# Performance work log

Hardware: AMD Instinct MI355X
Metric: run time of the kernel (lower is better)

Reference implementation:

```python
import jax, jax.numpy as jnp
import numpy as np
from jax.scipy.special import logsumexp

G, H, L, N, K = 2000, 128, 10, 4096, 10
TAU, LC, LA, EPS = 0.1, 1.0, 0.5, 1e-6

def _lin_init(k, fi, fo):
    return jax.random.normal(k, (fi, fo), jnp.float32) / np.sqrt(fi)

def setup_inputs():
    key = jax.random.key(0)
    ks = jax.random.split(key, 12)
    return {
        'wt_x': jax.random.normal(ks[0], (N, G), jnp.float32),
        'ko_x': jax.random.normal(ks[1], (N, G), jnp.float32),
        'wt_labels': jax.random.randint(ks[2], (N,), 0, K, dtype=jnp.int32),
        'ko_labels': jax.random.randint(ks[3], (N,), 0, K, dtype=jnp.int32),
        'enc_w1': _lin_init(ks[4], G, H), 'enc_b1': jnp.zeros((H,)),
        'enc_g': jnp.ones((H,)), 'enc_be': jnp.zeros((H,)),
        'enc_w2': _lin_init(ks[5], H, L), 'enc_b2': jnp.zeros((L,)),
        'kap_w1': _lin_init(ks[6], G, H), 'kap_b1': jnp.zeros((H,)),
        'kap_g': jnp.ones((H,)), 'kap_be': jnp.zeros((H,)),
        'kap_w2': _lin_init(ks[7], H, 1), 'kap_b2': jnp.zeros((1,)),
        'dec_w1': _lin_init(ks[8], L, H), 'dec_b1': jnp.zeros((H,)),
        'dec_g': jnp.ones((H,)), 'dec_be': jnp.zeros((H,)),
        'dec_w2': _lin_init(ks[9], H, G), 'dec_b2': jnp.zeros((G,)),
    }

def _mlp(x, w1, b1, g, be, w2, b2):
    # Linear -> LayerNorm -> ReLU -> Linear (dropout_prob=0)
    h = x @ w1 + b1
    m = h.mean(-1, keepdims=True)
    v = ((h - m) ** 2).mean(-1, keepdims=True)
    h = (h - m) / jnp.sqrt(v + 1e-5) * g + be
    return jax.nn.relu(h) @ w2 + b2

def _contrastive(z_wt, z_ko, y_wt, y_ko):
    S = (z_wt @ z_ko.T) / TAU  # [Nwt, Nko], unit-norm z so |S| <= 1/tau
    total = jnp.float32(0.0)
    n_shared = jnp.float32(0.0)
    for c in range(K):  # fixed small class count
        mwt = (y_wt == c).astype(S.dtype)
        mko = (y_ko == c).astype(S.dtype)
        n_wt, n_ko = mwt.sum(), mko.sum()
        valid = (n_wt > 0) & (n_ko > 0)
        nw, nk = jnp.maximum(n_wt, 1.0), jnp.maximum(n_ko, 1.0)
        # mean_{i in c, j in c} (LSE_i - S_ij) over ko columns of class c
        lse_r = logsumexp(jnp.where(mko[None, :] > 0, S, -1e4), axis=1)
        l1 = jnp.sum(mwt * (lse_r - (S @ mko) / nk)) / nw
        lse_c = logsumexp(jnp.where(mwt[:, None] > 0, S, -1e4), axis=0)
        l2 = jnp.sum(mko * (lse_c - (mwt @ S) / nw)) / nk
        total = total + jnp.where(valid, 0.5 * (l1 + l2), 0.0)
        n_shared = n_shared + valid.astype(S.dtype)
    return jnp.where(n_shared > 0, total / jnp.maximum(n_shared, 1.0), 0.0)

def _alignment(z, y):
    ones = jnp.ones(z.shape[0], z.dtype)
    counts = jax.ops.segment_sum(ones, y, num_segments=K)
    mu_c = jax.ops.segment_sum(z, y, num_segments=K) / jnp.maximum(counts, 1.0)[:, None]
    dev = z - mu_c[y]
    per_class = jax.ops.segment_sum(jnp.sum(dev ** 2, axis=1), y, num_segments=K) / jnp.maximum(counts, 1.0)
    present = counts > 0
    return jnp.sum(jnp.where(present, per_class, 0.0)) / jnp.maximum(jnp.sum(present.astype(z.dtype)), 1.0)

def reference(wt_x, ko_x, enc_w1, enc_b1, enc_g, enc_be, enc_w2, enc_b2, kap_w1, kap_b1, kap_g, kap_be, kap_w2, kap_b2, dec_w1, dec_b1, dec_g, dec_be, dec_w2, dec_b2, wt_labels, ko_labels):
    def encode(x):
        mu = _mlp(x, enc_w1, enc_b1, enc_g, enc_be, enc_w2, enc_b2)
        mu = mu / jnp.maximum(jnp.linalg.norm(mu, axis=1, keepdims=True), 1e-12)
        kappa = jax.nn.softplus(_mlp(x, kap_w1, kap_b1, kap_g, kap_be, kap_w2, kap_b2)) + EPS
        return mu, kappa
    wt_mu, wt_kappa = encode(wt_x)
    ko_mu, ko_kappa = encode(ko_x)
    wt_z, ko_z = wt_mu, ko_mu  # eval mode: z = mu (deterministic)
    wt_rec = _mlp(wt_z, dec_w1, dec_b1, dec_g, dec_be, dec_w2, dec_b2)
    ko_rec = _mlp(ko_z, dec_w1, dec_b1, dec_g, dec_be, dec_w2, dec_b2)
    recon = jnp.mean((wt_rec - wt_x) ** 2) + jnp.mean((ko_rec - ko_x) ** 2)
    kl = (wt_kappa.mean() + ko_kappa.mean()) * 0.01
    contrast = _contrastive(wt_z, ko_z, wt_labels, ko_labels)
    align = _alignment(jnp.concatenate([wt_z, ko_z], 0), jnp.concatenate([wt_labels, ko_labels], 0))
    return recon + kl + LC * contrast + LA * align
```

## Files before the change

kernel.cpp:

```cpp
#include <hip/hip_runtime.h>
#include <math.h>

typedef __attribute__((ext_vector_type(8))) __bf16 bf16x8;
typedef __attribute__((ext_vector_type(4))) float f32x4;

#define GL2LDS_(gptr, lptr) \
    __builtin_amdgcn_global_load_lds((const __attribute__((address_space(1))) void*)(gptr), \
                                     (__attribute__((address_space(3))) void*)(lptr), 16, 0, 0)

#define OFF_NWT   0
#define OFF_NKO   10
#define OFF_L1    20
#define OFF_L2    30
#define OFF_CNT   40
#define OFF_ZSUM  50
#define OFF_ZSQ   150
#define OFF_KSUM  160
#define OFF_REC   162
#define IOFF_WTOFF 192
#define IOFF_KOOFF 204
#define IOFF_WTCTR 216
#define IOFF_KOCTR 226
#define ACC_FLOATS 256

#define WT_OFF    256
#define WTLO_OFF  (WT_OFF + 262144)
#define H_OFF     (WTLO_OFF + 262144)
#define Z_OFF     (H_OFF + 8192*256)
#define KAP_OFF   (Z_OFF + 8192*10)
#define HREST_OFF (KAP_OFF + 8192)
#define HPART     2097152

#define ACT_HI_OFF  H_OFF
#define ACT_LO_OFF  (H_OFF + 524288)
#define BT_HI_OFF   (H_OFF + 1048576)
#define BT_LO_OFF   (H_OFF + 1179648)
#define ZCKO_OFF    (H_OFF + 1310720)
#define ZCWT_OFF    (H_OFF + 1351680)
#define PART_OFF    (H_OFF + 1392640)

__global__ __launch_bounds__(256) void pack_w_kernel(const float* __restrict__ enc_w1,
                                                     const float* __restrict__ kap_w1,
                                                     __bf16* __restrict__ WThi,
                                                     __bf16* __restrict__ WTlo)
{
    __shared__ float tile[64][65];
    int kt = blockIdx.x & 31;
    int ct = blockIdx.x >> 5;
    int k0 = kt * 64, c0 = ct * 64;
    int t = threadIdx.x;
    int lr = t >> 6, lc = t & 63;
#pragma unroll
    for (int i = 0; i < 16; ++i) {
        int k = k0 + lr + 4 * i;
        int c = c0 + lc;
        float v = 0.f;
        if (k < 2000) v = (c < 128) ? enc_w1[(size_t)k * 128 + c]
                                    : kap_w1[(size_t)k * 128 + (c - 128)];
        tile[lc][lr + 4 * i] = v;
    }
    __syncthreads();
#pragma unroll
    for (int i = 0; i < 16; ++i) {
        int c = c0 + lr + 4 * i;
        int k = k0 + lc;
        float v = tile[lr + 4 * i][lc];
        __bf16 h = (__bf16)v;
        __bf16 l = (__bf16)(v - (float)h);
        size_t idx = (size_t)c * 2048 + k;
        WThi[idx] = h;
        WTlo[idx] = l;
    }
}

__global__ __launch_bounds__(256) void pack_dw2_kernel(const float* __restrict__ dw2,
                                                       __bf16* __restrict__ BThi,
                                                       __bf16* __restrict__ BTlo)
{
    __shared__ float tile[64][129];
    int j0 = blockIdx.x * 64;
    int t = threadIdx.x;
#pragma unroll
    for (int i = 0; i < 32; ++i) {
        int idx = i * 256 + t;
        int c = idx >> 6, jj = idx & 63;
        int j = j0 + jj;
        tile[jj][c] = (j < 2000) ? dw2[(size_t)c * 2000 + j] : 0.f;
    }
    __syncthreads();
#pragma unroll
    for (int i = 0; i < 32; ++i) {
        int idx = i * 256 + t;
        int jj = idx >> 7, c = idx & 127;
        float v = tile[jj][c];
        __bf16 h = (__bf16)v;
        size_t o = (size_t)(j0 + jj) * 128 + c;
        BThi[o] = h;
        BTlo[o] = (__bf16)(v - (float)h);
    }
}

__global__ void counts_kernel(const int* __restrict__ wtl, const int* __restrict__ kol,
                              float* __restrict__ acc)
{
    __shared__ int cw[10], ck[10];
    int t = threadIdx.x;
    if (t < 10) { cw[t] = 0; ck[t] = 0; }
    __syncthreads();
    for (int i = t; i < 4096; i += 1024) {
        atomicAdd(&cw[wtl[i]], 1);
        atomicAdd(&ck[kol[i]], 1);
    }
    __syncthreads();
    if (t < 10) { acc[OFF_NWT + t] = (float)cw[t]; acc[OFF_NKO + t] = (float)ck[t]; }
    if (t == 0) {
        int* ai = (int*)acc;
        int aw = 0, ak = 0;
        for (int c = 0; c < 10; ++c) {
            ai[IOFF_WTOFF + c] = aw; aw += cw[c];
            ai[IOFF_KOOFF + c] = ak; ak += ck[c];
        }
        ai[IOFF_WTOFF + 10] = aw;
        ai[IOFF_KOOFF + 10] = ak;
    }
}

__global__ __launch_bounds__(256) void scatter_z_kernel(const float* __restrict__ Z,
                                                        const int* __restrict__ wtl,
                                                        const int* __restrict__ kol,
                                                        float* __restrict__ acc,
                                                        float* __restrict__ ZcWT,
                                                        float* __restrict__ ZcKO)
{
    __shared__ int lcnt[20];
    __shared__ int lbase[20];
    int t = threadIdx.x;
    if (t < 20) lcnt[t] = 0;
    __syncthreads();
    int row = blockIdx.x * 256 + t;
    int side = row >= 4096;
    int r = side ? row - 4096 : row;
    int c = side ? kol[r] : wtl[r];
    int key = side * 10 + c;
    int myrank = atomicAdd(&lcnt[key], 1);
    __syncthreads();
    int* ai = (int*)acc;
    if (t < 20 && lcnt[t] > 0)
        lbase[t] = atomicAdd(&ai[IOFF_WTCTR + t], lcnt[t]);
    __syncthreads();
    int off = side ? ai[IOFF_KOOFF + c] : ai[IOFF_WTOFF + c];
    int slot = off + lbase[key] + myrank;
    float* dst = side ? ZcKO : ZcWT;
    const float* zr = Z + (size_t)row * 10;
#pragma unroll
    for (int d = 0; d < 10; ++d) dst[d * 4096 + slot] = zr[d];
}

__global__ __launch_bounds__(512) void gemm1_kernel(const float* __restrict__ wt_x,
                                                    const float* __restrict__ ko_x,
                                                    const __bf16* __restrict__ WThi,
                                                    const __bf16* __restrict__ WTlo,
                                                    float* __restrict__ Hb,
                                                    float* __restrict__ Hrest,
                                                    int nkc)
{
    __shared__ short Bs[2][2][2][4096];
    int t = threadIdx.x;
    int widx = t >> 6, lane = t & 63;
    int wm = widx >> 1, wn = widx & 1;
    int b = blockIdx.x;
    int mt = b & 63, strip = (b >> 6) & 1, kc = b >> 7;
    int R0 = mt * 128;
    int cb = strip * 128;
    int kchunk = 2048 / nkc;
    int kbase = kc * kchunk;
    int kleft = 2000 - kbase;
    int nsteps = (kleft < kchunk) ? ((kleft + 31) >> 5) : (kchunk >> 5);
    int ntiles = (nsteps + 1) >> 1;

    const float* xb = (R0 < 4096) ? (wt_x + (size_t)R0 * 2000)
                                  : (ko_x + (size_t)(R0 - 4096) * 2000);
    int ar = wm * 32 + (lane & 15);
    const float* xrow0 = xb + (size_t)ar * 2000 + kbase;
    const float* xrow1 = xrow0 + (size_t)16 * 2000;
    int kboff = (lane >> 4) * 8;

    int col0 = t >> 2;
    int s0   = (t & 3) ^ ((col0 >> 1) & 3);
    size_t boff = (size_t)(cb + col0) * 2048 + kbase + s0 * 8;
    const __bf16* bsrcH = WThi + boff;
    const __bf16* bsrcL = WTlo + boff;

#define STAGEB_(buf, tl) do { \
    int st_ = (tl) * 2; \
    GL2LDS_(bsrcH + (size_t)st_ * 32,       &Bs[buf][0][0][t * 8]); \
    GL2LDS_(bsrcH + (size_t)(st_ + 1) * 32, &Bs[buf][0][1][t * 8]); \
    GL2LDS_(bsrcL + (size_t)st_ * 32,       &Bs[buf][1][0][t * 8]); \
    GL2LDS_(bsrcL + (size_t)(st_ + 1) * 32, &Bs[buf][1][1][t * 8]); } while (0)

    f32x4 acc00, acc01, acc02, acc03;
    f32x4 acc10, acc11, acc12, acc13;
#pragma unroll
    for (int r = 0; r < 4; ++r) {
        acc00[r]=0.f; acc01[r]=0.f; acc02[r]=0.f; acc03[r]=0.f;
        acc10[r]=0.f; acc11[r]=0.f; acc12[r]=0.f; acc13[r]=0.f;
    }

    float4 aA00, aA01, aA10, aA11, aA20, aA21, aA30, aA31;
    float4 aB00, aB01, aB10, aB11, aB20, aB21, aB30, aB31;

#define GLOADA_(step, a00, a01, a10, a11) do { \
    int k0_ = (step) * 32; \
    int k_ = k0_ + kboff; \
    if (kbase + k0_ <= 1952) { \
        a00 = *(const float4*)(xrow0 + k_); \
        a01 = *(const float4*)(xrow0 + k_ + 4); \
        a10 = *(const float4*)(xrow1 + k_); \
        a11 = *(const float4*)(xrow1 + k_ + 4); \
    } else { \
        float t0_[8], t1_[8]; \
        _Pragma("unroll") \
        for (int j = 0; j < 8; ++j) { \
            int kk = kbase + k_ + j; \
            t0_[j] = (kk < 2000) ? xrow0[k_ + j] : 0.f; \
            t1_[j] = (kk < 2000) ? xrow1[k_ + j] : 0.f; } \
        a00 = make_float4(t0_[0], t0_[1], t0_[2], t0_[3]); \
        a01 = make_float4(t0_[4], t0_[5], t0_[6], t0_[7]); \
        a10 = make_float4(t1_[0], t1_[1], t1_[2], t1_[3]); \
        a11 = make_float4(t1_[4], t1_[5], t1_[6], t1_[7]); } } while (0)

#define CONVA_(a0, a1, ahi, alo) do { \
    float av_[8] = {a0.x, a0.y, a0.z, a0.w, a1.x, a1.y, a1.z, a1.w}; \
    _Pragma("unroll") \
    for (int j = 0; j < 8; ++j) { \
        __bf16 h_ = (__bf16)av_[j]; \
        ahi[j] = h_; \
        alo[j] = (__bf16)(av_[j] - (float)h_); } } while (0)

#define MFMAH_(buf, half, ahi0, alo0, ahi1, alo1) do { \
    _Pragma("unroll") \
    for (int nf = 0; nf < 4; ++nf) { \
        bf16x8 bhf = *(const bf16x8*)&Bs[buf][0][half][(ubase + nf * 64) * 8]; \
        bf16x8 blf = *(const bf16x8*)&Bs[buf][1][half][(ubase + nf * 64) * 8]; \
        f32x4* a0 = (nf == 0) ? &acc00 : (nf == 1) ? &acc01 : (nf == 2) ? &acc02 : &acc03; \
        f32x4* a1 = (nf == 0) ? &acc10 : (nf == 1) ? &acc11 : (nf == 2) ? &acc12 : &acc13; \
        *a0 = __builtin_amdgcn_mfma_f32_16x16x32_bf16(ahi0, bhf, *a0, 0, 0, 0); \
        *a0 = __builtin_amdgcn_mfma_f32_16x16x32_bf16(alo0, bhf, *a0, 0, 0, 0); \
        *a0 = __builtin_amdgcn_mfma_f32_16x16x32_bf16(ahi0, blf, *a0, 0, 0, 0); \
        *a1 = __builtin_amdgcn_mfma_f32_16x16x32_bf16(ahi1, bhf, *a1, 0, 0, 0); \
        *a1 = __builtin_amdgcn_mfma_f32_16x16x32_bf16(alo1, bhf, *a1, 0, 0, 0); \
        *a1 = __builtin_amdgcn_mfma_f32_16x16x32_bf16(ahi1, blf, *a1, 0, 0, 0); } } while (0)

    STAGEB_(0, 0);
    GLOADA_(0, aA00, aA01, aA10, aA11);
    GLOADA_(1, aA20, aA21, aA30, aA31);
    if (1 < ntiles) {
        GLOADA_(2, aB00, aB01, aB10, aB11);
        GLOADA_(3, aB20, aB21, aB30, aB31);
    }
    __syncthreads();

    int cpr = lane & 15;
    int pph = (lane >> 4) ^ ((cpr >> 1) & 3);
    int ubase = (wn * 64 + cpr) * 4 + pph;

    int half_iters = (ntiles + 1) >> 1;
    for (int it = 0; it < half_iters; ++it) {
        int tl = it * 2;
        {
            if (tl + 1 < ntiles) STAGEB_(1, tl + 1);
            bf16x8 h00,l00,h01,l01,h10,l10,h11,l11;
            CONVA_(aA00, aA01, h00, l00); CONVA_(aA10, aA11, h01, l01);
            CONVA_(aA20, aA21, h10, l10); CONVA_(aA30, aA31, h11, l11);
            if (tl + 2 < ntiles) {
                GLOADA_(2*(tl+2),   aA00, aA01, aA10, aA11);
                GLOADA_(2*(tl+2)+1, aA20, aA21, aA30, aA31);
            }
            MFMAH_(0, 0, h00, l00, h01, l01);
            MFMAH_(0, 1, h10, l10, h11, l11);
            __syncthreads();
        }
        if (tl + 1 < ntiles) {
            if (tl + 2 < ntiles) STAGEB_(0, tl + 2);
            bf16x8 h00,l00,h01,l01,h10,l10,h11,l11;
            CONVA_(aB00, aB01, h00, l00); CONVA_(aB10, aB11, h01, l01);
            CONVA_(aB20, aB21, h10, l10); CONVA_(aB30, aB31, h11, l11);
            if (tl + 3 < ntiles) {
                GLOADA_(2*(tl+3),   aB00, aB01, aB10, aB11);
                GLOADA_(2*(tl+3)+1, aB20, aB21, aB30, aB31);
            }
            MFMAH_(1, 0, h00, l00, h01, l01);
            MFMAH_(1, 1, h10, l10, h11, l11);
            __syncthreads();
        }
    }

    float* Hq = (kc == 0) ? Hb : (Hrest + (size_t)(kc - 1) * HPART);
#pragma unroll
    for (int r = 0; r < 4; ++r) {
        int row0 = R0 + wm * 32 + (lane >> 4) * 4 + r;
        size_t base0 = (size_t)row0 * 256 + cb + wn * 64 + (lane & 15);
        Hq[base0]      = acc00[r];
        Hq[base0 + 16] = acc01[r];
        Hq[base0 + 32] = acc02[r];
        Hq[base0 + 48] = acc03[r];
        size_t base1 = base0 + (size_t)16 * 256;
        Hq[base1]      = acc10[r];
        Hq[base1 + 16] = acc11[r];
        Hq[base1 + 32] = acc12[r];
        Hq[base1 + 48] = acc13[r];
    }
#undef STAGEB_
#undef GLOADA_
#undef CONVA_
#undef MFMAH_
}

__global__ __launch_bounds__(128) void stage2_kernel(const float* __restrict__ Hb,
    const float* __restrict__ Hrest, int nkc,
    const float* __restrict__ enc_b1, const float* __restrict__ enc_g, const float* __restrict__ enc_be,
    const float* __restrict__ enc_w2, const float* __restrict__ enc_b2,
    const float* __restrict__ kap_b1, const float* __restrict__ kap_g, const float* __restrict__ kap_be,
    const float* __restrict__ kap_w2, const float* __restrict__ kap_b2,
    float* __restrict__ Z, float* __restrict__ Kap)
{
    __shared__ float sh[128];
    int row  = blockIdx.x;
    int wave = threadIdx.x >> 6;
    int lane = threadIdx.x & 63;
    size_t hoff = (size_t)row * 256 + wave * 128;
    const float* hb  = Hb + hoff;
    const float* b1 = wave ? kap_b1 : enc_b1;
    const float* gg = wave ? kap_g  : enc_g;
    const float* bb = wave ? kap_be : enc_be;

    float h0 = hb[lane]      + b1[lane];
    float h1 = hb[lane + 64] + b1[lane + 64];
    for (int j = 0; j + 1 < nkc; ++j) {
        const float* hr = Hrest + (size_t)j * HPART + hoff;
        h0 += hr[lane];
        h1 += hr[lane + 64];
    }
    float s = h0 + h1;
#pragma unroll
    for (int o = 32; o > 0; o >>= 1) s += __shfl_xor(s, o, 64);
    float m = s * (1.f / 128.f);
    float d0 = h0 - m, d1 = h1 - m;
    float v = d0 * d0 + d1 * d1;
#pragma unroll
    for (int o = 32; o > 0; o >>= 1) v += __shfl_xor(v, o, 64);
    v *= (1.f / 128.f);
    float sc = 1.f / sqrtf(v + 1e-5f);
    float r0 = fmaxf(fmaf(d0 * sc, gg[lane],      bb[lane]),      0.f);
    float r1 = fmaxf(fmaf(d1 * sc, gg[lane + 64], bb[lane + 64]), 0.f);

    if (wave == 0) { sh[lane] = r0; sh[lane + 64] = r1; }
    __syncthreads();

    if (wave == 0) {
        float mu = 0.f;
        if (lane < 10) {
            mu = enc_b2[lane];
            for (int c = 0; c < 128; ++c) mu = fmaf(sh[c], enc_w2[c * 10 + lane], mu);
        }
        float n2 = mu * mu;
#pragma unroll
        for (int o = 8; o > 0; o >>= 1) n2 += __shfl_xor(n2, o, 16);
        float inv = 1.f / fmaxf(sqrtf(n2), 1e-12f);
        if (lane < 10) Z[(size_t)row * 10 + lane] = mu * inv;
    } else {
        float p = r0 * kap_w2[lane] + r1 * kap_w2[lane + 64];
#pragma unroll
        for (int o = 32; o > 0; o >>= 1) p += __shfl_xor(p, o, 64);
        if (lane == 0) {
            float x = p + kap_b2[0];
            float sp = (x > 20.f) ? x : log1pf(expf(x));
            Kap[row] = sp + 1e-6f;
        }
    }
}

__global__ __launch_bounds__(256) void dec_act_kernel(const float* __restrict__ Zb,
    const float* __restrict__ dw1, const float* __restrict__ db1,
    const float* __restrict__ dg,  const float* __restrict__ dbe,
    __bf16* __restrict__ Ahi, __bf16* __restrict__ Alo)
{
    int wave = threadIdx.x >> 6;
    int lane = threadIdx.x & 63;
    int row = blockIdx.x * 4 + wave;
    const float* zr = Zb + (size_t)row * 10;
    float z[10];
#pragma unroll
    for (int d = 0; d < 10; ++d) z[d] = zr[d];
    int c0 = lane, c1 = lane + 64;
    float h0 = db1[c0], h1 = db1[c1];
#pragma unroll
    for (int d = 0; d < 10; ++d) {
        h0 = fmaf(z[d], dw1[d * 128 + c0], h0);
        h1 = fmaf(z[d], dw1[d * 128 + c1], h1);
    }
    float s = h0 + h1;
#pragma unroll
    for (int o = 32; o > 0; o >>= 1) s += __shfl_xor(s, o, 64);
    float m = s * (1.f / 128.f);
    float d0 = h0 - m, d1 = h1 - m;
    float v = d0 * d0 + d1 * d1;
#pragma unroll
    for (int o = 32; o > 0; o >>= 1) v += __shfl_xor(v, o, 64);
    v *= (1.f / 128.f);
    float sc = 1.f / sqrtf(v + 1e-5f);
    float a0 = fmaxf(fmaf(d0 * sc, dg[c0], dbe[c0]), 0.f);
    float a1 = fmaxf(fmaf(d1 * sc, dg[c1], dbe[c1]), 0.f);
    __bf16 h0b = (__bf16)a0, h1b = (__bf16)a1;
    size_t base = (size_t)row * 128;
    Ahi[base + c0] = h0b;                 Ahi[base + c1] = h1b;
    Alo[base + c0] = (__bf16)(a0 - (float)h0b);
    Alo[base + c1] = (__bf16)(a1 - (float)h1b);
}

__global__ __launch_bounds__(512, 4) void dec_gemm_kernel(
    const __bf16* __restrict__ Ahi, const __bf16* __restrict__ Alo,
    const __bf16* __restrict__ BThi, const __bf16* __restrict__ BTlo,
    const float* __restrict__ wt_x, const float* __restrict__ ko_x,
    const float* __restrict__ db2, float* __restrict__ acc)
{
    __shared__ short BsH[2][8192];
    __shared__ short BsL[2][8192];
    __shared__ float rs[8];
    int t = threadIdx.x;
    int widx = t >> 6, lane = t & 63;
    int wm = widx >> 2, wn = widx & 3;
    int R0 = (blockIdx.x >> 1) * 32;
    int T0 = (blockIdx.x & 1) * 16;
    const float* xbase = (R0 < 4096) ? wt_x : ko_x;
    int xr0 = ((R0 < 4096) ? R0 : R0 - 4096) + wm * 16 + (lane >> 4) * 4;

    size_t abase = (size_t)(R0 + wm * 16 + (lane & 15)) * 128 + (lane >> 4) * 8;
    bf16x8 ah0 = *(const bf16x8*)(Ahi + abase);
    bf16x8 ah1 = *(const bf16x8*)(Ahi + abase + 32);
    bf16x8 ah2 = *(const bf16x8*)(Ahi + abase + 64);
    bf16x8 ah3 = *(const bf16x8*)(Ahi + abase + 96);
    bf16x8 al0 = *(const bf16x8*)(Alo + abase);
    bf16x8 al1 = *(const bf16x8*)(Alo + abase + 32);
    bf16x8 al2 = *(const bf16x8*)(Alo + abase + 64);
    bf16x8 al3 = *(const bf16x8*)(Alo + abase + 96);

    int g0c = t >> 4,         g0s = t & 15;
    int g1c = (t + 512) >> 4, g1s = t & 15;
    int u0 = g0c * 16 + (g0s ^ (g0c & 7));
    int u1 = g1c * 16 + (g1s ^ (g1c & 7));

    int col_local = wn * 16 + (lane & 15);
    int cl7 = col_local & 7;
    int rb = col_local * 16;
    int sb = lane >> 4;

    uint4 hA0, hA1, lA0, lA1, hB0, hB1, lB0, lB1;

#define GLOADB_(tile, h0, h1, l0, l1) do { \
    size_t gb = (size_t)(tile) * 8192; \
    h0 = *(const uint4*)(BThi + gb + (size_t)t * 8); \
    h1 = *(const uint4*)(BThi + gb + (size_t)(t + 512) * 8); \
    l0 = *(const uint4*)(BTlo + gb + (size_t)t * 8); \
    l1 = *(const uint4*)(BTlo + gb + (size_t)(t + 512) * 8); } while (0)

#define DSWRITE_(buf, h0, h1, l0, l1) do { \
    *(uint4*)&BsH[buf][u0 * 8] = h0; \
    *(uint4*)&BsH[buf][u1 * 8] = h1; \
    *(uint4*)&BsL[buf][u0 * 8] = l0; \
    *(uint4*)&BsL[buf][u1 * 8] = l1; } while (0)

#define COMPUTE_(buf, tile) do { \
    int un0 = rb + ((sb +  0) ^ cl7); \
    int un1 = rb + ((sb +  4) ^ cl7); \
    int un2 = rb + ((sb +  8) ^ cl7); \
    int un3 = rb + ((sb + 12) ^ cl7); \
    bf16x8 bh0 = *(const bf16x8*)&BsH[buf][un0 * 8]; \
    bf16x8 bh1 = *(const bf16x8*)&BsH[buf][un1 * 8]; \
    bf16x8 bh2 = *(const bf16x8*)&BsH[buf][un2 * 8]; \
    bf16x8 bh3 = *(const bf16x8*)&BsH[buf][un3 * 8]; \
    bf16x8 bl0 = *(const bf16x8*)&BsL[buf][un0 * 8]; \
    bf16x8 bl1 = *(const bf16x8*)&BsL[buf][un1 * 8]; \
    bf16x8 bl2 = *(const bf16x8*)&BsL[buf][un2 * 8]; \
    bf16x8 bl3 = *(const bf16x8*)&BsL[buf][un3 * 8]; \
    f32x4 a4; \
    _Pragma("unroll") \
    for (int r = 0; r < 4; ++r) a4[r] = 0.f; \
    a4 = __builtin_amdgcn_mfma_f32_16x16x32_bf16(ah0, bh0, a4, 0, 0, 0); \
    a4 = __builtin_amdgcn_mfma_f32_16x16x32_bf16(al0, bh0, a4, 0, 0, 0); \
    a4 = __builtin_amdgcn_mfma_f32_16x16x32_bf16(ah0, bl0, a4, 0, 0, 0); \
    a4 = __builtin_amdgcn_mfma_f32_16x16x32_bf16(ah1, bh1, a4, 0, 0, 0); \
    a4 = __builtin_amdgcn_mfma_f32_16x16x32_bf16(al1, bh1, a4, 0, 0, 0); \
    a4 = __builtin_amdgcn_mfma_f32_16x16x32_bf16(ah1, bl1, a4, 0, 0, 0); \
    a4 = __builtin_amdgcn_mfma_f32_16x16x32_bf16(ah2, bh2, a4, 0, 0, 0); \
    a4 = __builtin_amdgcn_mfma_f32_16x16x32_bf16(al2, bh2, a4, 0, 0, 0); \
    a4 = __builtin_amdgcn_mfma_f32_16x16x32_bf16(ah2, bl2, a4, 0, 0, 0); \
    a4 = __builtin_amdgcn_mfma_f32_16x16x32_bf16(ah3, bh3, a4, 0, 0, 0); \
    a4 = __builtin_amdgcn_mfma_f32_16x16x32_bf16(al3, bh3, a4, 0, 0, 0); \
    a4 = __builtin_amdgcn_mfma_f32_16x16x32_bf16(ah3, bl3, a4, 0, 0, 0); \
    int col = (tile) * 64 + col_local; \
    if (col < 2000) { \
        float bb = db2[col]; \
        _Pragma("unroll") \
        for (int r = 0; r < 4; ++r) { \
            float xv = xbase[(size_t)(xr0 + r) * 2000 + col]; \
            float e = a4[r] + bb - xv; \
            rsum = fmaf(e, e, rsum); \
        } } } while (0)

    float rsum = 0.f;
    GLOADB_(T0 + 0, hA0, hA1, lA0, lA1);
    GLOADB_(T0 + 1, hB0, hB1, lB0, lB1);
    DSWRITE_(0, hA0, hA1, lA0, lA1);
    __syncthreads();

    for (int it = 0; it < 8; ++it) {
        int lt = it * 2;
        {
            if (lt + 2 < 16) GLOADB_(T0 + lt + 2, hA0, hA1, lA0, lA1);
            DSWRITE_(1, hB0, hB1, lB0, lB1);
            COMPUTE_(0, T0 + lt);
            __syncthreads();
        }
        {
            if (lt + 3 < 16) GLOADB_(T0 + lt + 3, hB0, hB1, lB0, lB1);
            if (lt + 2 < 16) DSWRITE_(0, hA0, hA1, lA0, lA1);
            COMPUTE_(1, T0 + lt + 1);
            __syncthreads();
        }
    }

#pragma unroll
    for (int o = 32; o > 0; o >>= 1) rsum += __shfl_xor(rsum, o, 64);
    if (lane == 0) rs[widx] = rsum;
    __syncthreads();
    if (t == 0) {
        float s = 0.f;
#pragma unroll
        for (int w = 0; w < 8; ++w) s += rs[w];
        atomicAdd(&acc[OFF_REC], s);
    }
#undef GLOADB_
#undef DSWRITE_
#undef COMPUTE_
}

#define MAXNB 768
__global__ __launch_bounds__(256) void contrast_kernel(const float* __restrict__ ZcWT,
                                                       const float* __restrict__ ZcKO,
                                                       float* __restrict__ acc)
{
    __shared__ float zb[MAXNB * 12];
    __shared__ float bsum[4];
    int b = blockIdx.x;
    int cs = b / 3, sub = b - cs * 3;
    int c = cs >> 1, side = cs & 1;
    const int* ai = (const int*)acc;
    int aStart = side ? ai[IOFF_KOOFF + c]     : ai[IOFF_WTOFF + c];
    int aEnd   = side ? ai[IOFF_KOOFF + c + 1] : ai[IOFF_WTOFF + c + 1];
    int bStart = side ? ai[IOFF_WTOFF + c]     : ai[IOFF_KOOFF + c];
    int bEnd   = side ? ai[IOFF_WTOFF + c + 1] : ai[IOFF_KOOFF + c + 1];
    int na = aEnd - aStart;
    int nb = bEnd - bStart;
    if (nb > MAXNB) nb = MAXNB;
    const float* ZA = side ? ZcKO : ZcWT;
    const float* ZB = side ? ZcWT : ZcKO;
    int t = threadIdx.x;

    for (int u = t; u < nb; u += 256) {
#pragma unroll
        for (int d = 0; d < 10; ++d) zb[u * 12 + d] = ZB[d * 4096 + bStart + u];
    }
    __syncthreads();

    int chunk = (na + 2) / 3;
    int r0 = sub * chunk;
    int rcnt = na - r0; if (rcnt > chunk) rcnt = chunk;

    float wsum = 0.f;
    bool waveActive = (nb > 0) && ((t & ~63) < rcnt);
    if (waveActive) {
        bool valid = t < rcnt;
        int ar = aStart + (valid ? (r0 + t) : 0);
        float za[10];
#pragma unroll
        for (int d = 0; d < 10; ++d) za[d] = ZA[d * 4096 + ar];
        float se = 0.f, ss = 0.f;
        for (int u = 0; u < nb; ++u) {
            const float* zp = &zb[u * 12];
            float s = 0.f;
#pragma unroll
            for (int d = 0; d < 10; ++d) s = fmaf(za[d], zp[d], s);
            s *= 10.f;
            se += __expf(s - 10.f);
            ss += s;
        }
        if (valid) wsum = (10.f + __logf(se)) - ss / (float)nb;
    }
#pragma unroll
    for (int o = 32; o > 0; o >>= 1) wsum += __shfl_xor(wsum, o, 64);
    if ((t & 63) == 0) bsum[t >> 6] = wsum;
    __syncthreads();
    if (t == 0) {
        float s = bsum[0] + bsum[1] + bsum[2] + bsum[3];
        if (s != 0.f || nb > 0)
            atomicAdd(&acc[(side ? OFF_L2 : OFF_L1) + c], s);
    }
}

__global__ __launch_bounds__(256) void align_kernel(const float* __restrict__ Z,
                                                    const int* __restrict__ wtl,
                                                    const int* __restrict__ kol,
                                                    const float* __restrict__ Kap,
                                                    float* __restrict__ Part)
{
    __shared__ float cL[10], qL[10], sL[100], ks;
    int t = threadIdx.x;
    if (t < 10) { cL[t] = 0.f; qL[t] = 0.f; }
    if (t < 100) sL[t] = 0.f;
    if (t == 0) ks = 0.f;
    __syncthreads();
    int row = blockIdx.x * 256 + t;
    int c = (row < 4096) ? wtl[row] : kol[row - 4096];
    float zz[10]; float q = 0.f;
#pragma unroll
    for (int d = 0; d < 10; ++d) { zz[d] = Z[(size_t)row * 10 + d]; q = fmaf(zz[d], zz[d], q); }
    atomicAdd(&cL[c], 1.f);
    atomicAdd(&qL[c], q);
#pragma unroll
    for (int d = 0; d < 10; ++d) atomicAdd(&sL[c * 10 + d], zz[d]);
    atomicAdd(&ks, Kap[row]);
    __syncthreads();
    float* pb = Part + (size_t)blockIdx.x * 128;
    if (t < 10)  { pb[t] = cL[t]; pb[10 + t] = qL[t]; }
    if (t < 100) pb[20 + t] = sL[t];
    if (t == 0)  pb[120] = ks;
}

__global__ void finalize_kernel(const float* __restrict__ Part,
                                const float* __restrict__ acc,
                                float* __restrict__ out)
{
    __shared__ float red[121];
    int t = threadIdx.x;
    if (t < 120) {
        float s = 0.f;
        for (int b = 0; b < 32; ++b) s += Part[(size_t)b * 128 + t];
        red[t] = s;
    } else if (t == 120) {
        float s = 0.f;
        for (int b = 0; b < 32; ++b) s += Part[(size_t)b * 128 + 120];
        red[120] = s;
    }
    __syncthreads();
    if (t == 0) {
        float total = 0.f, nsh = 0.f;
        for (int c = 0; c < 10; ++c) {
            float nw = acc[OFF_NWT + c], nk = acc[OFF_NKO + c];
            if (nw > 0.5f && nk > 0.5f) {
                float l1 = acc[OFF_L1 + c] / nw;
                float l2 = acc[OFF_L2 + c] / nk;
                total += 0.5f * (l1 + l2);
                nsh += 1.f;
            }
        }
        float contrast = (nsh > 0.f) ? total / nsh : 0.f;
        float ap = 0.f, np_ = 0.f;
        for (int c = 0; c < 10; ++c) {
            float cn = red[c];
            if (cn > 0.5f) {
                float mu2 = 0.f;
                for (int d = 0; d < 10; ++d) {
                    float mm = red[20 + c * 10 + d] / cn;
                    mu2 = fmaf(mm, mm, mu2);
                }
                ap += red[10 + c] / cn - mu2;
                np_ += 1.f;
            }
        }
        float align = (np_ > 0.f) ? ap / np_ : 0.f;
        float kl = 0.01f * red[120] * (1.f / 4096.f);
        float recon = acc[OFF_REC] * (1.f / 8192000.f);
        out[0] = recon + kl + 1.0f * contrast + 0.5f * align;
    }
}

extern "C" void kernel_launch(void* const* d_in, const int* in_sizes, int n_in,
                              void* d_out, int out_size, void* d_ws, size_t ws_size,
                              hipStream_t stream)
{
    const float* wt_x   = (const float*)d_in[0];
    const float* ko_x   = (const float*)d_in[1];
    const int*   wtl    = (const int*)d_in[2];
    const int*   kol    = (const int*)d_in[3];
    const float* enc_w1 = (const float*)d_in[4];
    const float* enc_b1 = (const float*)d_in[5];
    const float* enc_g  = (const float*)d_in[6];
    const float* enc_be = (const float*)d_in[7];
    const float* enc_w2 = (const float*)d_in[8];
    const float* enc_b2 = (const float*)d_in[9];
    const float* kap_w1 = (const float*)d_in[10];
    const float* kap_b1 = (const float*)d_in[11];
    const float* kap_g  = (const float*)d_in[12];
    const float* kap_be = (const float*)d_in[13];
    const float* kap_w2 = (const float*)d_in[14];
    const float* kap_b2 = (const float*)d_in[15];
    const float* dw1    = (const float*)d_in[16];
    const float* db1    = (const float*)d_in[17];
    const float* dg     = (const float*)d_in[18];
    const float* dbe    = (const float*)d_in[19];
    const float* dw2    = (const float*)d_in[20];
    const float* db2    = (const float*)d_in[21];

    float* ws  = (float*)d_ws;
    float* acc = ws;
    __bf16* WThi = (__bf16*)(ws + WT_OFF);
    __bf16* WTlo = (__bf16*)(ws + WTLO_OFF);
    float* Hb    = ws + H_OFF;
    float* Zb    = ws + Z_OFF;
    float* Kap   = ws + KAP_OFF;
    float* Hrest = ws + HREST_OFF;
    __bf16* Ahi  = (__bf16*)(ws + ACT_HI_OFF);
    __bf16* Alo  = (__bf16*)(ws + ACT_LO_OFF);
    __bf16* BThi = (__bf16*)(ws + BT_HI_OFF);
    __bf16* BTlo = (__bf16*)(ws + BT_LO_OFF);
    float* ZcKO = ws + ZCKO_OFF;
    float* ZcWT = ws + ZCWT_OFF;
    float* Part = ws + PART_OFF;

    size_t need4 = (size_t)(HREST_OFF + 3 * HPART) * sizeof(float);
    int nkc = (ws_size >= need4) ? 4 : 2;

    hipMemsetAsync(acc, 0, ACC_FLOATS * sizeof(float), stream);
    pack_w_kernel<<<128, 256, 0, stream>>>(enc_w1, kap_w1, WThi, WTlo);
    counts_kernel<<<1, 1024, 0, stream>>>(wtl, kol, acc);
    gemm1_kernel<<<128 * nkc, 512, 0, stream>>>(wt_x, ko_x, WThi, WTlo, Hb, Hrest, nkc);
    stage2_kernel<<<8192, 128, 0, stream>>>(Hb, Hrest, nkc, enc_b1, enc_g, enc_be, enc_w2, enc_b2,
                                            kap_b1, kap_g, kap_be, kap_w2, kap_b2, Zb, Kap);
    pack_dw2_kernel<<<32, 256, 0, stream>>>(dw2, BThi, BTlo);
    dec_act_kernel<<<2048, 256, 0, stream>>>(Zb, dw1, db1, dg, dbe, Ahi, Alo);
    scatter_z_kernel<<<32, 256, 0, stream>>>(Zb, wtl, kol, acc, ZcWT, ZcKO);
    contrast_kernel<<<60, 256, 0, stream>>>(ZcWT, ZcKO, acc);
    align_kernel<<<32, 256, 0, stream>>>(Zb, wtl, kol, Kap, Part);
    dec_gemm_kernel<<<512, 512, 0, stream>>>(Ahi, Alo, BThi, BTlo, wt_x, ko_x, db2, acc);
    finalize_kernel<<<1, 128, 0, stream>>>(Part, acc, (float*)d_out);
}
```

Measured before the change: 174.5 us.

## Add 8-way split-K encoder GEMM and fuse decoder activation and scatter/align kernels

Adds a split-K=8 variant of the first encoder GEMM that stages its whole 256-wide K slice of B into LDS in one go, giving 1024 blocks for better occupancy. It is chosen when the workspace is large enough. The decoder first-layer LayerNorm/ReLU activation is fused into stage2, so the separate dec_act pass that re-read Z is gone. The scatter and alignment-partial kernels are merged into one launch. The costs are more partial H buffers for stage2 to sum, and a workspace layout that moves the tail buffers past the extra partials.

```diff
diff --git a/kernel.cpp b/kernel.cpp
--- a/kernel.cpp
+++ b/kernel.cpp
@@ -12,32 +12,19 @@
 #define OFF_NKO   10
 #define OFF_L1    20
 #define OFF_L2    30
-#define OFF_CNT   40
-#define OFF_ZSUM  50
-#define OFF_ZSQ   150
-#define OFF_KSUM  160
 #define OFF_REC   162
 #define IOFF_WTOFF 192
 #define IOFF_KOOFF 204
 #define IOFF_WTCTR 216
-#define IOFF_KOCTR 226
 #define ACC_FLOATS 256
 
 #define WT_OFF    256
 #define WTLO_OFF  (WT_OFF + 262144)
 #define H_OFF     (WTLO_OFF + 262144)
-#define Z_OFF     (H_OFF + 8192*256)
-#define KAP_OFF   (Z_OFF + 8192*10)
+#define Z_OFF     (H_OFF + 2097152)
+#define KAP_OFF   (Z_OFF + 81920)
 #define HREST_OFF (KAP_OFF + 8192)
 #define HPART     2097152
-
-#define ACT_HI_OFF  H_OFF
-#define ACT_LO_OFF  (H_OFF + 524288)
-#define BT_HI_OFF   (H_OFF + 1048576)
-#define BT_LO_OFF   (H_OFF + 1179648)
-#define ZCKO_OFF    (H_OFF + 1310720)
-#define ZCWT_OFF    (H_OFF + 1351680)
-#define PART_OFF    (H_OFF + 1392640)
 
 __global__ __launch_bounds__(256) void pack_w_kernel(const float* __restrict__ enc_w1,
                                                      const float* __restrict__ kap_w1,
@@ -125,46 +112,14 @@
     }
 }
 
-__global__ __launch_bounds__(256) void scatter_z_kernel(const float* __restrict__ Z,
-                                                        const int* __restrict__ wtl,
-                                                        const int* __restrict__ kol,
-                                                        float* __restrict__ acc,
-                                                        float* __restrict__ ZcWT,
-                                                        float* __restrict__ ZcKO)
-{
-    __shared__ int lcnt[20];
-    __shared__ int lbase[20];
-    int t = threadIdx.x;
-    if (t < 20) lcnt[t] = 0;
-    __syncthreads();
-    int row = blockIdx.x * 256 + t;
-    int side = row >= 4096;
-    int r = side ? row - 4096 : row;
-    int c = side ? kol[r] : wtl[r];
-    int key = side * 10 + c;
-    int myrank = atomicAdd(&lcnt[key], 1);
-    __syncthreads();
-    int* ai = (int*)acc;
-    if (t < 20 && lcnt[t] > 0)
-        lbase[t] = atomicAdd(&ai[IOFF_WTCTR + t], lcnt[t]);
-    __syncthreads();
-    int off = side ? ai[IOFF_KOOFF + c] : ai[IOFF_WTOFF + c];
-    int slot = off + lbase[key] + myrank;
-    float* dst = side ? ZcKO : ZcWT;
-    const float* zr = Z + (size_t)row * 10;
-#pragma unroll
-    for (int d = 0; d < 10; ++d) dst[d * 4096 + slot] = zr[d];
-}
-
-__global__ __launch_bounds__(512) void gemm1_kernel(const float* __restrict__ wt_x,
-                                                    const float* __restrict__ ko_x,
-                                                    const __bf16* __restrict__ WThi,
-                                                    const __bf16* __restrict__ WTlo,
-                                                    float* __restrict__ Hb,
-                                                    float* __restrict__ Hrest,
-                                                    int nkc)
-{
-    __shared__ short Bs[2][2][2][4096];
+__global__ __launch_bounds__(512) void gemm1_mono_kernel(const float* __restrict__ wt_x,
+                                                         const float* __restrict__ ko_x,
+                                                         const __bf16* __restrict__ WThi,
+                                                         const __bf16* __restrict__ WTlo,
+                                                         float* __restrict__ Hb,
+                                                         float* __restrict__ Hrest)
+{
+    __shared__ short Bs[2][8][4096];
     int t = threadIdx.x;
     int widx = t >> 6, lane = t & 63;
     int wm = widx >> 1, wn = widx & 1;
@@ -172,11 +127,9 @@
     int mt = b & 63, strip = (b >> 6) & 1, kc = b >> 7;
     int R0 = mt * 128;
     int cb = strip * 128;
-    int kchunk = 2048 / nkc;
-    int kbase = kc * kchunk;
+    int kbase = kc * 256;
     int kleft = 2000 - kbase;
-    int nsteps = (kleft < kchunk) ? ((kleft + 31) >> 5) : (kchunk >> 5);
-    int ntiles = (nsteps + 1) >> 1;
+    int nsteps = (kleft < 256) ? ((kleft + 31) >> 5) : 8;
 
     const float* xb = (R0 < 4096) ? (wt_x + (size_t)R0 * 2000)
                                   : (ko_x + (size_t)(R0 - 4096) * 2000);
@@ -191,12 +144,11 @@
     const __bf16* bsrcH = WThi + boff;
     const __bf16* bsrcL = WTlo + boff;
 
-#define STAGEB_(buf, tl) do { \
-    int st_ = (tl) * 2; \
-    GL2LDS_(bsrcH + (size_t)st_ * 32,       &Bs[buf][0][0][t * 8]); \
-    GL2LDS_(bsrcH + (size_t)(st_ + 1) * 32, &Bs[buf][0][1][t * 8]); \
-    GL2LDS_(bsrcL + (size_t)st_ * 32,       &Bs[buf][1][0][t * 8]); \
-    GL2LDS_(bsrcL + (size_t)(st_ + 1) * 32, &Bs[buf][1][1][t * 8]); } while (0)
+#pragma unroll
+    for (int s = 0; s < 8; ++s) {
+        GL2LDS_(bsrcH + (size_t)s * 32, &Bs[0][s][t * 8]);
+        GL2LDS_(bsrcL + (size_t)s * 32, &Bs[1][s][t * 8]);
+    }
 
     f32x4 acc00, acc01, acc02, acc03;
     f32x4 acc10, acc11, acc12, acc13;
@@ -206,8 +158,8 @@
         acc10[r]=0.f; acc11[r]=0.f; acc12[r]=0.f; acc13[r]=0.f;
     }
 
-    float4 aA00, aA01, aA10, aA11, aA20, aA21, aA30, aA31;
-    float4 aB00, aB01, aB10, aB11, aB20, aB21, aB30, aB31;
+    float4 aA00, aA01, aA10, aA11;
+    float4 aB00, aB01, aB10, aB11;
 
 #define GLOADA_(step, a00, a01, a10, a11) do { \
     int k0_ = (step) * 32; \
@@ -237,6 +189,148 @@
         ahi[j] = h_; \
         alo[j] = (__bf16)(av_[j] - (float)h_); } } while (0)
 
+#define MFMAS_(step, ahi0, alo0, ahi1, alo1) do { \
+    _Pragma("unroll") \
+    for (int nf = 0; nf < 4; ++nf) { \
+        bf16x8 bhf = *(const bf16x8*)&Bs[0][step][(ubase + nf * 64) * 8]; \
+        bf16x8 blf = *(const bf16x8*)&Bs[1][step][(ubase + nf * 64) * 8]; \
+        f32x4* a0 = (nf == 0) ? &acc00 : (nf == 1) ? &acc01 : (nf == 2) ? &acc02 : &acc03; \
+        f32x4* a1 = (nf == 0) ? &acc10 : (nf == 1) ? &acc11 : (nf == 2) ? &acc12 : &acc13; \
+        *a0 = __builtin_amdgcn_mfma_f32_16x16x32_bf16(ahi0, bhf, *a0, 0, 0, 0); \
+        *a0 = __builtin_amdgcn_mfma_f32_16x16x32_bf16(alo0, bhf, *a0, 0, 0, 0); \
+        *a0 = __builtin_amdgcn_mfma_f32_16x16x32_bf16(ahi0, blf, *a0, 0, 0, 0); \
+        *a1 = __builtin_amdgcn_mfma_f32_16x16x32_bf16(ahi1, bhf, *a1, 0, 0, 0); \
+        *a1 = __builtin_amdgcn_mfma_f32_16x16x32_bf16(alo1, bhf, *a1, 0, 0, 0); \
+        *a1 = __builtin_amdgcn_mfma_f32_16x16x32_bf16(ahi1, blf, *a1, 0, 0, 0); } } while (0)
+
+    GLOADA_(0, aA00, aA01, aA10, aA11);
+    if (1 < nsteps) GLOADA_(1, aB00, aB01, aB10, aB11);
+    __syncthreads();
+
+    int cpr = lane & 15;
+    int pph = (lane >> 4) ^ ((cpr >> 1) & 3);
+    int ubase = (wn * 64 + cpr) * 4 + pph;
+
+#pragma unroll
+    for (int p = 0; p < 4; ++p) {
+        int st0 = 2 * p, st1 = 2 * p + 1;
+        if (st0 < nsteps) {
+            bf16x8 h0, l0, h1, l1;
+            CONVA_(aA00, aA01, h0, l0);
+            CONVA_(aA10, aA11, h1, l1);
+            if (st0 + 2 < nsteps) GLOADA_(st0 + 2, aA00, aA01, aA10, aA11);
+            MFMAS_(st0, h0, l0, h1, l1);
+        }
+        if (st1 < nsteps) {
+            bf16x8 h0, l0, h1, l1;
+            CONVA_(aB00, aB01, h0, l0);
+            CONVA_(aB10, aB11, h1, l1);
+            if (st1 + 2 < nsteps) GLOADA_(st1 + 2, aB00, aB01, aB10, aB11);
+            MFMAS_(st1, h0, l0, h1, l1);
+        }
+    }
+
+    float* Hq = (kc == 0) ? Hb : (Hrest + (size_t)(kc - 1) * HPART);
+#pragma unroll
+    for (int r = 0; r < 4; ++r) {
+        int row0 = R0 + wm * 32 + (lane >> 4) * 4 + r;
+        size_t base0 = (size_t)row0 * 256 + cb + wn * 64 + (lane & 15);
+        Hq[base0]      = acc00[r];
+        Hq[base0 + 16] = acc01[r];
+        Hq[base0 + 32] = acc02[r];
+        Hq[base0 + 48] = acc03[r];
+        size_t base1 = base0 + (size_t)16 * 256;
+        Hq[base1]      = acc10[r];
+        Hq[base1 + 16] = acc11[r];
+        Hq[base1 + 32] = acc12[r];
+        Hq[base1 + 48] = acc13[r];
+    }
+#undef GLOADA_
+#undef CONVA_
+#undef MFMAS_
+}
+
+__global__ __launch_bounds__(512) void gemm1_kernel(const float* __restrict__ wt_x,
+                                                    const float* __restrict__ ko_x,
+                                                    const __bf16* __restrict__ WThi,
+                                                    const __bf16* __restrict__ WTlo,
+                                                    float* __restrict__ Hb,
+                                                    float* __restrict__ Hrest,
+                                                    int nkc)
+{
+    __shared__ short Bs[2][2][2][4096];
+    int t = threadIdx.x;
+    int widx = t >> 6, lane = t & 63;
+    int wm = widx >> 1, wn = widx & 1;
+    int b = blockIdx.x;
+    int mt = b & 63, strip = (b >> 6) & 1, kc = b >> 7;
+    int R0 = mt * 128;
+    int cb = strip * 128;
+    int kchunk = 2048 / nkc;
+    int kbase = kc * kchunk;
+    int kleft = 2000 - kbase;
+    int nsteps = (kleft < kchunk) ? ((kleft + 31) >> 5) : (kchunk >> 5);
+    int ntiles = (nsteps + 1) >> 1;
+
+    const float* xb = (R0 < 4096) ? (wt_x + (size_t)R0 * 2000)
+                                  : (ko_x + (size_t)(R0 - 4096) * 2000);
+    int ar = wm * 32 + (lane & 15);
+    const float* xrow0 = xb + (size_t)ar * 2000 + kbase;
+    const float* xrow1 = xrow0 + (size_t)16 * 2000;
+    int kboff = (lane >> 4) * 8;
+
+    int col0 = t >> 2;
+    int s0   = (t & 3) ^ ((col0 >> 1) & 3);
+    size_t boff = (size_t)(cb + col0) * 2048 + kbase + s0 * 8;
+    const __bf16* bsrcH = WThi + boff;
+    const __bf16* bsrcL = WTlo + boff;
+
+#define STAGEB_(buf, tl) do { \
+    int st_ = (tl) * 2; \
+    GL2LDS_(bsrcH + (size_t)st_ * 32,       &Bs[buf][0][0][t * 8]); \
+    GL2LDS_(bsrcH + (size_t)(st_ + 1) * 32, &Bs[buf][0][1][t * 8]); \
+    GL2LDS_(bsrcL + (size_t)st_ * 32,       &Bs[buf][1][0][t * 8]); \
+    GL2LDS_(bsrcL + (size_t)(st_ + 1) * 32, &Bs[buf][1][1][t * 8]); } while (0)
+
+    f32x4 acc00, acc01, acc02, acc03;
+    f32x4 acc10, acc11, acc12, acc13;
+#pragma unroll
+    for (int r = 0; r < 4; ++r) {
+        acc00[r]=0.f; acc01[r]=0.f; acc02[r]=0.f; acc03[r]=0.f;
+        acc10[r]=0.f; acc11[r]=0.f; acc12[r]=0.f; acc13[r]=0.f;
+    }
+
+    float4 aA00, aA01, aA10, aA11, aA20, aA21, aA30, aA31;
+    float4 aB00, aB01, aB10, aB11, aB20, aB21, aB30, aB31;
+
+#define GLOADA_(step, a00, a01, a10, a11) do { \
+    int k0_ = (step) * 32; \
+    int k_ = k0_ + kboff; \
+    if (kbase + k0_ <= 1952) { \
+        a00 = *(const float4*)(xrow0 + k_); \
+        a01 = *(const float4*)(xrow0 + k_ + 4); \
+        a10 = *(const float4*)(xrow1 + k_); \
+        a11 = *(const float4*)(xrow1 + k_ + 4); \
+    } else { \
+        float t0_[8], t1_[8]; \
+        _Pragma("unroll") \
+        for (int j = 0; j < 8; ++j) { \
+            int kk = kbase + k_ + j; \
+            t0_[j] = (kk < 2000) ? xrow0[k_ + j] : 0.f; \
+            t1_[j] = (kk < 2000) ? xrow1[k_ + j] : 0.f; } \
+        a00 = make_float4(t0_[0], t0_[1], t0_[2], t0_[3]); \
+        a01 = make_float4(t0_[4], t0_[5], t0_[6], t0_[7]); \
+        a10 = make_float4(t1_[0], t1_[1], t1_[2], t1_[3]); \
+        a11 = make_float4(t1_[4], t1_[5], t1_[6], t1_[7]); } } while (0)
+
+#define CONVA_(a0, a1, ahi, alo) do { \
+    float av_[8] = {a0.x, a0.y, a0.z, a0.w, a1.x, a1.y, a1.z, a1.w}; \
+    _Pragma("unroll") \
+    for (int j = 0; j < 8; ++j) { \
+        __bf16 h_ = (__bf16)av_[j]; \
+        ahi[j] = h_; \
+        alo[j] = (__bf16)(av_[j] - (float)h_); } } while (0)
+
 #define MFMAH_(buf, half, ahi0, alo0, ahi1, alo1) do { \
     _Pragma("unroll") \
     for (int nf = 0; nf < 4; ++nf) { \
@@ -322,9 +416,14 @@
     const float* __restrict__ enc_w2, const float* __restrict__ enc_b2,
     const float* __restrict__ kap_b1, const float* __restrict__ kap_g, const float* __restrict__ kap_be,
     const float* __restrict__ kap_w2, const float* __restrict__ kap_b2,
-    float* __restrict__ Z, float* __restrict__ Kap)
+    const float* __restrict__ dw1, const float* __restrict__ db1,
+    const float* __restrict__ dg,  const float* __restrict__ dbe,
+    float* __restrict__ Z, float* __restrict__ Kap,
+    __bf16* __restrict__ Ahi, __bf16* __restrict__ Alo)
 {
     __shared__ float sh[128];
+    __shared__ float shz[10];
+    __shared__ float dred[2], dvar[2];
     int row  = blockIdx.x;
     int wave = threadIdx.x >> 6;
     int lane = threadIdx.x & 63;
@@ -367,7 +466,11 @@
 #pragma unroll
         for (int o = 8; o > 0; o >>= 1) n2 += __shfl_xor(n2, o, 16);
         float inv = 1.f / fmaxf(sqrtf(n2), 1e-12f);
-        if (lane < 10) Z[(size_t)row * 10 + lane] = mu * inv;
+        if (lane < 10) {
+            float zv = mu * inv;
+            Z[(size_t)row * 10 + lane] = zv;
+            shz[lane] = zv;
+        }
     } else {
         float p = r0 * kap_w2[lane] + r1 * kap_w2[lane + 64];
 #pragma unroll
@@ -378,44 +481,85 @@
             Kap[row] = sp + 1e-6f;
         }
     }
-}
-
-__global__ __launch_bounds__(256) void dec_act_kernel(const float* __restrict__ Zb,
-    const float* __restrict__ dw1, const float* __restrict__ db1,
-    const float* __restrict__ dg,  const float* __restrict__ dbe,
-    __bf16* __restrict__ Ahi, __bf16* __restrict__ Alo)
-{
-    int wave = threadIdx.x >> 6;
-    int lane = threadIdx.x & 63;
-    int row = blockIdx.x * 4 + wave;
-    const float* zr = Zb + (size_t)row * 10;
-    float z[10];
-#pragma unroll
-    for (int d = 0; d < 10; ++d) z[d] = zr[d];
-    int c0 = lane, c1 = lane + 64;
-    float h0 = db1[c0], h1 = db1[c1];
-#pragma unroll
-    for (int d = 0; d < 10; ++d) {
-        h0 = fmaf(z[d], dw1[d * 128 + c0], h0);
-        h1 = fmaf(z[d], dw1[d * 128 + c1], h1);
-    }
-    float s = h0 + h1;
-#pragma unroll
-    for (int o = 32; o > 0; o >>= 1) s += __shfl_xor(s, o, 64);
-    float m = s * (1.f / 128.f);
-    float d0 = h0 - m, d1 = h1 - m;
-    float v = d0 * d0 + d1 * d1;
-#pragma unroll
-    for (int o = 32; o > 0; o >>= 1) v += __shfl_xor(v, o, 64);
-    v *= (1.f / 128.f);
-    float sc = 1.f / sqrtf(v + 1e-5f);
-    float a0 = fmaxf(fmaf(d0 * sc, dg[c0], dbe[c0]), 0.f);
-    float a1 = fmaxf(fmaf(d1 * sc, dg[c1], dbe[c1]), 0.f);
-    __bf16 h0b = (__bf16)a0, h1b = (__bf16)a1;
-    size_t base = (size_t)row * 128;
-    Ahi[base + c0] = h0b;                 Ahi[base + c1] = h1b;
-    Alo[base + c0] = (__bf16)(a0 - (float)h0b);
-    Alo[base + c1] = (__bf16)(a1 - (float)h1b);
+    __syncthreads();
+
+    {
+        float z[10];
+#pragma unroll
+        for (int d = 0; d < 10; ++d) z[d] = shz[d];
+        int c = threadIdx.x;
+        float h = db1[c];
+#pragma unroll
+        for (int d = 0; d < 10; ++d) h = fmaf(z[d], dw1[d * 128 + c], h);
+        float s2 = h;
+#pragma unroll
+        for (int o = 32; o > 0; o >>= 1) s2 += __shfl_xor(s2, o, 64);
+        if (lane == 0) dred[wave] = s2;
+        __syncthreads();
+        float m2 = (dred[0] + dred[1]) * (1.f / 128.f);
+        float dd = h - m2;
+        float v2 = dd * dd;
+#pragma unroll
+        for (int o = 32; o > 0; o >>= 1) v2 += __shfl_xor(v2, o, 64);
+        if (lane == 0) dvar[wave] = v2;
+        __syncthreads();
+        float var = (dvar[0] + dvar[1]) * (1.f / 128.f);
+        float sc2 = 1.f / sqrtf(var + 1e-5f);
+        float a = fmaxf(fmaf(dd * sc2, dg[c], dbe[c]), 0.f);
+        __bf16 hb_ = (__bf16)a;
+        size_t base = (size_t)row * 128 + c;
+        Ahi[base] = hb_;
+        Alo[base] = (__bf16)(a - (float)hb_);
+    }
+}
+
+__global__ __launch_bounds__(256) void scatter_align_kernel(const float* __restrict__ Z,
+                                                            const int* __restrict__ wtl,
+                                                            const int* __restrict__ kol,
+                                                            const float* __restrict__ Kap,
+                                                            float* __restrict__ acc,
+                                                            float* __restrict__ ZcWT,
+                                                            float* __restrict__ ZcKO,
+                                                            float* __restrict__ Part)
+{
+    __shared__ int lcnt[20];
+    __shared__ int lbase[20];
+    __shared__ float cL[10], qL[10], sL[100], ks;
+    int t = threadIdx.x;
+    if (t < 20) lcnt[t] = 0;
+    if (t < 10) { cL[t] = 0.f; qL[t] = 0.f; }
+    if (t >= 20 && t < 120) sL[t - 20] = 0.f;
+    if (t == 120) ks = 0.f;
+    __syncthreads();
+    int row = blockIdx.x * 256 + t;
+    int side = row >= 4096;
+    int r = side ? row - 4096 : row;
+    int c = side ? kol[r] : wtl[r];
+    int key = side * 10 + c;
+    int myrank = atomicAdd(&lcnt[key], 1);
+    float zz[10]; float q = 0.f;
+    const float* zr = Z + (size_t)row * 10;
+#pragma unroll
+    for (int d = 0; d < 10; ++d) { zz[d] = zr[d]; q = fmaf(zz[d], zz[d], q); }
+    atomicAdd(&cL[c], 1.f);
+    atomicAdd(&qL[c], q);
+#pragma unroll
+    for (int d = 0; d < 10; ++d) atomicAdd(&sL[c * 10 + d], zz[d]);
+    atomicAdd(&ks, Kap[row]);
+    __syncthreads();
+    int* ai = (int*)acc;
+    if (t < 20 && lcnt[t] > 0)
+        lbase[t] = atomicAdd(&ai[IOFF_WTCTR + t], lcnt[t]);
+    __syncthreads();
+    int off = side ? ai[IOFF_KOOFF + c] : ai[IOFF_WTOFF + c];
+    int slot = off + lbase[key] + myrank;
+    float* dst = side ? ZcKO : ZcWT;
+#pragma unroll
+    for (int d = 0; d < 10; ++d) dst[d * 4096 + slot] = zz[d];
+    float* pb = Part + (size_t)blockIdx.x * 128;
+    if (t < 10)  { pb[t] = cL[t]; pb[10 + t] = qL[t]; }
+    if (t < 100) pb[20 + t] = sL[t];
+    if (t == 0)  pb[120] = ks;
 }
 
 __global__ __launch_bounds__(512, 4) void dec_gemm_kernel(
@@ -608,35 +752,6 @@
     }
 }
 
-__global__ __launch_bounds__(256) void align_kernel(const float* __restrict__ Z,
-                                                    const int* __restrict__ wtl,
-                                                    const int* __restrict__ kol,
-                                                    const float* __restrict__ Kap,
-                                                    float* __restrict__ Part)
-{
-    __shared__ float cL[10], qL[10], sL[100], ks;
-    int t = threadIdx.x;
-    if (t < 10) { cL[t] = 0.f; qL[t] = 0.f; }
-    if (t < 100) sL[t] = 0.f;
-    if (t == 0) ks = 0.f;
-    __syncthreads();
-    int row = blockIdx.x * 256 + t;
-    int c = (row < 4096) ? wtl[row] : kol[row - 4096];
-    float zz[10]; float q = 0.f;
-#pragma unroll
-    for (int d = 0; d < 10; ++d) { zz[d] = Z[(size_t)row * 10 + d]; q = fmaf(zz[d], zz[d], q); }
-    atomicAdd(&cL[c], 1.f);
-    atomicAdd(&qL[c], q);
-#pragma unroll
-    for (int d = 0; d < 10; ++d) atomicAdd(&sL[c * 10 + d], zz[d]);
-    atomicAdd(&ks, Kap[row]);
-    __syncthreads();
-    float* pb = Part + (size_t)blockIdx.x * 128;
-    if (t < 10)  { pb[t] = cL[t]; pb[10 + t] = qL[t]; }
-    if (t < 100) pb[20 + t] = sL[t];
-    if (t == 0)  pb[120] = ks;
-}
-
 __global__ void finalize_kernel(const float* __restrict__ Part,
                                 const float* __restrict__ acc,
                                 float* __restrict__ out)
@@ -720,28 +835,37 @@
     float* Zb    = ws + Z_OFF;
     float* Kap   = ws + KAP_OFF;
     float* Hrest = ws + HREST_OFF;
-    __bf16* Ahi  = (__bf16*)(ws + ACT_HI_OFF);
-    __bf16* Alo  = (__bf16*)(ws + ACT_LO_OFF);
-    __bf16* BThi = (__bf16*)(ws + BT_HI_OFF);
-    __bf16* BTlo = (__bf16*)(ws + BT_LO_OFF);
-    float* ZcKO = ws + ZCKO_OFF;
-    float* ZcWT = ws + ZCWT_OFF;
-    float* Part = ws + PART_OFF;
-
-    size_t need4 = (size_t)(HREST_OFF + 3 * HPART) * sizeof(float);
-    int nkc = (ws_size >= need4) ? 4 : 2;
+
+    const size_t TAIL = 2 * 524288 + 2 * 131072 + 2 * 40960 + 4096;
+    size_t need8 = (size_t)(HREST_OFF + 7 * HPART + TAIL) * sizeof(float);
+    size_t need4 = (size_t)(HREST_OFF + 3 * HPART + TAIL) * sizeof(float);
+    int nkc; bool mono;
+    if (ws_size >= need8)      { nkc = 8; mono = true;  }
+    else if (ws_size >= need4) { nkc = 4; mono = false; }
+    else                       { nkc = 2; mono = false; }
+
+    float* tail = ws + HREST_OFF + (size_t)(nkc - 1) * HPART;
+    __bf16* Ahi  = (__bf16*)tail;
+    __bf16* Alo  = (__bf16*)(tail + 524288);
+    __bf16* BThi = (__bf16*)(tail + 1048576);
+    __bf16* BTlo = (__bf16*)(tail + 1048576 + 131072);
+    float* ZcKO = tail + 1048576 + 262144;
+    float* ZcWT = ZcKO + 40960;
+    float* Part = ZcWT + 40960;
 
     hipMemsetAsync(acc, 0, ACC_FLOATS * sizeof(float), stream);
     pack_w_kernel<<<128, 256, 0, stream>>>(enc_w1, kap_w1, WThi, WTlo);
     counts_kernel<<<1, 1024, 0, stream>>>(wtl, kol, acc);
-    gemm1_kernel<<<128 * nkc, 512, 0, stream>>>(wt_x, ko_x, WThi, WTlo, Hb, Hrest, nkc);
+    if (mono)
+        gemm1_mono_kernel<<<1024, 512, 0, stream>>>(wt_x, ko_x, WThi, WTlo, Hb, Hrest);
+    else
+        gemm1_kernel<<<128 * nkc, 512, 0, stream>>>(wt_x, ko_x, WThi, WTlo, Hb, Hrest, nkc);
     stage2_kernel<<<8192, 128, 0, stream>>>(Hb, Hrest, nkc, enc_b1, enc_g, enc_be, enc_w2, enc_b2,
-                                            kap_b1, kap_g, kap_be, kap_w2, kap_b2, Zb, Kap);
+                                            kap_b1, kap_g, kap_be, kap_w2, kap_b2,
+                                            dw1, db1, dg, dbe, Zb, Kap, Ahi, Alo);
     pack_dw2_kernel<<<32, 256, 0, stream>>>(dw2, BThi, BTlo);
-    dec_act_kernel<<<2048, 256, 0, stream>>>(Zb, dw1, db1, dg, dbe, Ahi, Alo);
-    scatter_z_kernel<<<32, 256, 0, stream>>>(Zb, wtl, kol, acc, ZcWT, ZcKO);
+    scatter_align_kernel<<<32, 256, 0, stream>>>(Zb, wtl, kol, Kap, acc, ZcWT, ZcKO, Part);
     contrast_kernel<<<60, 256, 0, stream>>>(ZcWT, ZcKO, acc);
-    align_kernel<<<32, 256, 0, stream>>>(Zb, wtl, kol, Kap, Part);
     dec_gemm_kernel<<<512, 512, 0, stream>>>(Ahi, Alo, BThi, BTlo, wt_x, ko_x, db2, acc);
     finalize_kernel<<<1, 128, 0, stream>>>(Part, acc, (float*)d_out);
 }
```

New measurement: 178.3 us. +2.2%, slower.
